# Optimization experiments

Hardware: AMD Instinct MI355X
Metric: run time of the kernel (lower is better)

Reference implementation:

```python
import jax, jax.numpy as jnp
import numpy as np

NEG_SLOPE = 0.2  # PyG GATConv default LeakyReLU slope
EPS = 1e-16


def gat_layer(x, W, a_src, a_dst, bias, src, dst, heads, out_dim, concat):
    N = x.shape[0]
    h = (x @ W).reshape(N, heads, out_dim)          # [N,H,C]
    alpha_src = (h * a_src).sum(-1)                  # [N,H]
    alpha_dst = (h * a_dst).sum(-1)                  # [N,H]
    e = jax.nn.leaky_relu(alpha_src[src] + alpha_dst[dst], NEG_SLOPE)  # [E,H]
    # segment softmax over incoming edges of each destination node
    m = jax.ops.segment_max(e, dst, num_segments=N)  # [N,H]
    p = jnp.exp(e - m[dst])
    denom = jax.ops.segment_sum(p, dst, num_segments=N)
    alpha = p / (denom[dst] + EPS)                   # [E,H]
    # scatter-aggregate messages to destinations
    out = jax.ops.segment_sum(alpha[:, :, None] * h[src], dst, num_segments=N)  # [N,H,C]
    out = out.reshape(N, heads * out_dim) if concat else out.mean(axis=1)
    return out + bias


def setup_inputs() -> dict:
    N, E, F_IN, NC = 100000, 1600000, 512, 10
    key = jax.random.key(0)
    ks = jax.random.split(key, 9)
    return {
        "x": jax.random.normal(ks[0], (N, F_IN), jnp.float32),
        "W1": jax.random.normal(ks[1], (F_IN, 64), jnp.float32) * (1.0 / np.sqrt(F_IN)),
        "att_src1": jax.random.normal(ks[2], (1, 8, 8), jnp.float32) * 0.1,
        "att_dst1": jax.random.normal(ks[3], (1, 8, 8), jnp.float32) * 0.1,
        "b1": jnp.zeros((64,), jnp.float32),
        "W2": jax.random.normal(ks[4], (64, NC), jnp.float32) * (1.0 / 8.0),
        "att_src2": jax.random.normal(ks[5], (1, 1, NC), jnp.float32) * 0.1,
        "att_dst2": jax.random.normal(ks[6], (1, 1, NC), jnp.float32) * 0.1,
        "b2": jnp.zeros((NC,), jnp.float32),
        "edge_index": jax.random.randint(ks[7], (2, E), 0, N, jnp.int64),
    }


def reference(x, W1, att_src1, att_dst1, b1, W2, att_src2, att_dst2, b2, edge_index):
    N = x.shape[0]
    # add self-loops (PyG GATConv add_self_loops=True default)
    loop = jnp.arange(N, dtype=edge_index.dtype)
    src = jnp.concatenate([edge_index[0], loop])
    dst = jnp.concatenate([edge_index[1], loop])
    h = gat_layer(x, W1, att_src1, att_dst1, b1, src, dst, heads=8, out_dim=8, concat=True)
    h = jax.nn.elu(h)
    nc = W2.shape[1]
    out = gat_layer(h, W2, att_src2, att_dst2, b2, src, dst, heads=1, out_dim=nc, concat=False)
    return jax.nn.log_softmax(out, axis=1)
```

## Files before the change

kernel.cpp:

```cpp
#include <hip/hip_runtime.h>
#include <math.h>

#define NEG 0.2f

typedef __bf16 bf16x8 __attribute__((ext_vector_type(8)));
typedef float  f32x4  __attribute__((ext_vector_type(4)));

__global__ void w1prep_k(const float* __restrict__ W1, __bf16* __restrict__ W1b)
{
    int i = blockIdx.x * 256 + threadIdx.x;
    int n = i & 63;
    int k0 = (i >> 6) * 8;
#pragma unroll
    for (int j = 0; j < 8; ++j)
        W1b[(size_t)i * 8 + j] = (__bf16)W1[(size_t)(k0 + j) * 64 + n];
}

__global__ __launch_bounds__(256, 4) void gemm1_k(const float* __restrict__ x,
                                                  const __bf16* __restrict__ W1b,
                                                  float* __restrict__ h1, int Nn)
{
    int t = threadIdx.x;
    int wave = t >> 6, lane = t & 63;
    int lm = lane & 15, lk = lane >> 4;
    int rowa = blockIdx.x * 64 + wave * 16 + lm;
    const float* xrow = x + (size_t)(rowa < Nn ? rowa : 0) * 512;
    f32x4 acc[4] = {};
#pragma unroll
    for (int ch = 0; ch < 16; ++ch) {
        float4 a0 = *(const float4*)(xrow + ch * 32 + lk * 8);
        float4 a1 = *(const float4*)(xrow + ch * 32 + lk * 8 + 4);
        bf16x8 af;
        af[0] = (__bf16)a0.x; af[1] = (__bf16)a0.y;
        af[2] = (__bf16)a0.z; af[3] = (__bf16)a0.w;
        af[4] = (__bf16)a1.x; af[5] = (__bf16)a1.y;
        af[6] = (__bf16)a1.z; af[7] = (__bf16)a1.w;
#pragma unroll
        for (int nt = 0; nt < 4; ++nt) {
            bf16x8 bf = *(const bf16x8*)(W1b + ((size_t)((ch * 4 + lk) * 64) + nt * 16 + lm) * 8);
            acc[nt] = __builtin_amdgcn_mfma_f32_16x16x32_bf16(af, bf, acc[nt], 0, 0, 0);
        }
    }
    int rowbase = blockIdx.x * 64 + wave * 16 + lk * 4;
#pragma unroll
    for (int nt = 0; nt < 4; ++nt) {
#pragma unroll
        for (int j = 0; j < 4; ++j) {
            int gr = rowbase + j;
            if (gr < Nn) h1[(size_t)gr * 64 + nt * 16 + lm] = acc[nt][j];
        }
    }
}

__global__ void attn1_k(const float* __restrict__ h1, const float* __restrict__ asrc,
                        const float* __restrict__ adst, float* __restrict__ as1,
                        float* __restrict__ ad1, int Nn)
{
    int tid = blockIdx.x * 256 + threadIdx.x;
    if (tid >= Nn * 8) return;
    int n = tid >> 3, h = tid & 7;
    const float* hp = h1 + (size_t)n * 64 + h * 8;
    float s = 0.f, d = 0.f;
#pragma unroll
    for (int c = 0; c < 8; ++c) {
        float v = hp[c];
        s += v * asrc[h * 8 + c];
        d += v * adst[h * 8 + c];
    }
    as1[tid] = s;
    ad1[tid] = d;
}

__global__ void hist_rank_k(const int* __restrict__ ei, int E, int Nn,
                            int* __restrict__ deg, int* __restrict__ rank)
{
    int e = blockIdx.x * 256 + threadIdx.x;
    int Ep = E + Nn;
    if (e >= Ep) return;
    int d = (e < E) ? ei[E + e] : e - E;
    rank[e] = atomicAdd(&deg[d], 1);
}

__global__ void scan_a_k(const int* __restrict__ deg, int Nn, int* __restrict__ bsum)
{
    __shared__ int tmp[256];
    int t = threadIdx.x;
    int base = blockIdx.x * 1024 + t * 4;
    int s = 0;
#pragma unroll
    for (int j = 0; j < 4; ++j) { int i = base + j; if (i < Nn) s += deg[i]; }
    tmp[t] = s;
    __syncthreads();
    for (int off = 1; off < 256; off <<= 1) {
        int a = (t >= off) ? tmp[t - off] : 0;
        __syncthreads();
        tmp[t] += a;
        __syncthreads();
    }
    if (t == 255) bsum[blockIdx.x] = tmp[255];
}

__global__ void scan_b_k(int* __restrict__ bsum, int nb)
{
    __shared__ int tmp[256];
    int t = threadIdx.x;
    int v = (t < nb) ? bsum[t] : 0;
    tmp[t] = v;
    __syncthreads();
    for (int off = 1; off < 256; off <<= 1) {
        int a = (t >= off) ? tmp[t - off] : 0;
        __syncthreads();
        tmp[t] += a;
        __syncthreads();
    }
    if (t < nb) bsum[t] = tmp[t] - v;
}

__global__ void scan_c_k(const int* __restrict__ deg, int Nn, const int* __restrict__ boff,
                         int* __restrict__ rowptr)
{
    __shared__ int tmp[256];
    int t = threadIdx.x;
    int base = blockIdx.x * 1024 + t * 4;
    int v[4];
    int s = 0;
#pragma unroll
    for (int j = 0; j < 4; ++j) {
        int i = base + j;
        v[j] = (i < Nn) ? deg[i] : 0;
        s += v[j];
    }
    tmp[t] = s;
    __syncthreads();
    for (int off = 1; off < 256; off <<= 1) {
        int a = (t >= off) ? tmp[t - off] : 0;
        __syncthreads();
        tmp[t] += a;
        __syncthreads();
    }
    int excl = boff[blockIdx.x] + tmp[t] - s;
#pragma unroll
    for (int j = 0; j < 4; ++j) {
        int i = base + j;
        if (i < Nn) {
            rowptr[i] = excl;
            excl += v[j];
            if (i == Nn - 1) rowptr[Nn] = excl;
        }
    }
}

__global__ void scat2_k(const int* __restrict__ ei, int E, int Nn,
                        const int* __restrict__ rowptr, const int* __restrict__ rank,
                        int* __restrict__ csr)
{
    int e = blockIdx.x * 256 + threadIdx.x;
    int Ep = E + Nn;
    if (e >= Ep) return;
    int s, d;
    if (e < E) { s = ei[e]; d = ei[E + e]; } else { s = d = e - E; }
    csr[rowptr[d] + rank[e]] = s;
}

__global__ __launch_bounds__(256) void agg1_k(const int* __restrict__ csr,
                                              const int* __restrict__ rowptr,
                                              const float* __restrict__ as1,
                                              const float* __restrict__ ad1,
                                              const float* __restrict__ h1,
                                              float* __restrict__ out1, int Nn)
{
    int wid = (blockIdx.x * 256 + threadIdx.x) >> 6;
    if (wid >= Nn) return;
    int lane = threadIdx.x & 63;
    int sub = lane >> 4;
    int c4 = lane & 15;
    int h = c4 >> 1;
    float adv = ad1[wid * 8 + h];
    int start = rowptr[wid];
    int len = rowptr[wid + 1] - start;
    float accp = 0.f;
    float4 accv = make_float4(0.f, 0.f, 0.f, 0.f);
    int i = sub;
    for (; i + 12 < len; i += 16) {
        int s0 = csr[start + i];
        int s1 = csr[start + i + 4];
        int s2 = csr[start + i + 8];
        int s3 = csr[start + i + 12];
        float e0 = as1[s0 * 8 + h] + adv;
        float e1 = as1[s1 * 8 + h] + adv;
        float e2 = as1[s2 * 8 + h] + adv;
        float e3 = as1[s3 * 8 + h] + adv;
        float4 hv0 = *(const float4*)(h1 + (size_t)s0 * 64 + c4 * 4);
        float4 hv1 = *(const float4*)(h1 + (size_t)s1 * 64 + c4 * 4);
        float4 hv2 = *(const float4*)(h1 + (size_t)s2 * 64 + c4 * 4);
        float4 hv3 = *(const float4*)(h1 + (size_t)s3 * 64 + c4 * 4);
        e0 = e0 > 0.f ? e0 : NEG * e0;
        e1 = e1 > 0.f ? e1 : NEG * e1;
        e2 = e2 > 0.f ? e2 : NEG * e2;
        e3 = e3 > 0.f ? e3 : NEG * e3;
        float p0 = __expf(e0), p1 = __expf(e1), p2 = __expf(e2), p3 = __expf(e3);
        accp += (p0 + p1) + (p2 + p3);
        accv.x += p0 * hv0.x + p1 * hv1.x + p2 * hv2.x + p3 * hv3.x;
        accv.y += p0 * hv0.y + p1 * hv1.y + p2 * hv2.y + p3 * hv3.y;
        accv.z += p0 * hv0.z + p1 * hv1.z + p2 * hv2.z + p3 * hv3.z;
        accv.w += p0 * hv0.w + p1 * hv1.w + p2 * hv2.w + p3 * hv3.w;
    }
    for (; i < len; i += 4) {
        int s0 = csr[start + i];
        float e0 = as1[s0 * 8 + h] + adv;
        float4 hv0 = *(const float4*)(h1 + (size_t)s0 * 64 + c4 * 4);
        e0 = e0 > 0.f ? e0 : NEG * e0;
        float p0 = __expf(e0);
        accp += p0;
        accv.x += p0 * hv0.x;
        accv.y += p0 * hv0.y;
        accv.z += p0 * hv0.z;
        accv.w += p0 * hv0.w;
    }
    accp   += __shfl_xor(accp, 16);
    accv.x += __shfl_xor(accv.x, 16);
    accv.y += __shfl_xor(accv.y, 16);
    accv.z += __shfl_xor(accv.z, 16);
    accv.w += __shfl_xor(accv.w, 16);
    accp   += __shfl_xor(accp, 32);
    accv.x += __shfl_xor(accv.x, 32);
    accv.y += __shfl_xor(accv.y, 32);
    accv.z += __shfl_xor(accv.z, 32);
    accv.w += __shfl_xor(accv.w, 32);
    if (sub == 0) {
        float inv = 1.f / (accp + 1e-16f);
        float4 o = make_float4(accv.x * inv, accv.y * inv, accv.z * inv, accv.w * inv);
        *(float4*)(out1 + (size_t)wid * 64 + c4 * 4) = o;
    }
}

__global__ void node2_k(const float* __restrict__ out1, const float* __restrict__ b1,
                        const float* __restrict__ W2, const float* __restrict__ as2w,
                        const float* __restrict__ ad2w, float* __restrict__ h2,
                        float* __restrict__ as2, float* __restrict__ ad2, int Nn)
{
    int n = blockIdx.x * 256 + threadIdx.x;
    if (n >= Nn) return;
    float g[64];
#pragma unroll
    for (int c = 0; c < 16; ++c) {
        float4 v = *(const float4*)(out1 + (size_t)n * 64 + c * 4);
        float4 b = *(const float4*)(b1 + c * 4);
        float t0 = v.x + b.x, t1 = v.y + b.y, t2 = v.z + b.z, t3 = v.w + b.w;
        g[c * 4 + 0] = t0 > 0.f ? t0 : expm1f(t0);
        g[c * 4 + 1] = t1 > 0.f ? t1 : expm1f(t1);
        g[c * 4 + 2] = t2 > 0.f ? t2 : expm1f(t2);
        g[c * 4 + 3] = t3 > 0.f ? t3 : expm1f(t3);
    }
    float acc[10] = {};
#pragma unroll
    for (int k = 0; k < 64; ++k) {
#pragma unroll
        for (int j = 0; j < 10; ++j) acc[j] += g[k] * W2[k * 10 + j];
    }
    float s = 0.f, d = 0.f;
#pragma unroll
    for (int j = 0; j < 10; ++j) {
        h2[(size_t)n * 16 + j] = acc[j];
        s += acc[j] * as2w[j];
        d += acc[j] * ad2w[j];
    }
    as2[n] = s;
    ad2[n] = d;
}

__global__ __launch_bounds__(256) void agg2_k(const int* __restrict__ csr,
                                              const int* __restrict__ rowptr,
                                              const float* __restrict__ as2,
                                              const float* __restrict__ ad2,
                                              const float* __restrict__ h2,
                                              float* __restrict__ out, int Nn)
{
    int wid = (blockIdx.x * 256 + threadIdx.x) >> 6;
    if (wid >= Nn) return;
    int lane = threadIdx.x & 63;
    int sub = lane >> 4;
    int c = lane & 15;
    float adv = ad2[wid];
    int start = rowptr[wid];
    int len = rowptr[wid + 1] - start;
    float accp = 0.f, accv = 0.f;
    int i = sub;
    for (; i + 12 < len; i += 16) {
        int s0 = csr[start + i];
        int s1 = csr[start + i + 4];
        int s2 = csr[start + i + 8];
        int s3 = csr[start + i + 12];
        float e0 = as2[s0] + adv;
        float e1 = as2[s1] + adv;
        float e2 = as2[s2] + adv;
        float e3 = as2[s3] + adv;
        float v0 = (c < 10) ? h2[(size_t)s0 * 16 + c] : 0.f;
        float v1 = (c < 10) ? h2[(size_t)s1 * 16 + c] : 0.f;
        float v2 = (c < 10) ? h2[(size_t)s2 * 16 + c] : 0.f;
        float v3 = (c < 10) ? h2[(size_t)s3 * 16 + c] : 0.f;
        e0 = e0 > 0.f ? e0 : NEG * e0;
        e1 = e1 > 0.f ? e1 : NEG * e1;
        e2 = e2 > 0.f ? e2 : NEG * e2;
        e3 = e3 > 0.f ? e3 : NEG * e3;
        float p0 = __expf(e0), p1 = __expf(e1), p2 = __expf(e2), p3 = __expf(e3);
        accp += (p0 + p1) + (p2 + p3);
        accv += p0 * v0 + p1 * v1 + p2 * v2 + p3 * v3;
    }
    for (; i < len; i += 4) {
        int s0 = csr[start + i];
        float e0 = as2[s0] + adv;
        float v0 = (c < 10) ? h2[(size_t)s0 * 16 + c] : 0.f;
        e0 = e0 > 0.f ? e0 : NEG * e0;
        float p0 = __expf(e0);
        accp += p0;
        accv += p0 * v0;
    }
    accp += __shfl_xor(accp, 16);
    accv += __shfl_xor(accv, 16);
    accp += __shfl_xor(accp, 32);
    accv += __shfl_xor(accv, 32);
    if (sub == 0 && c < 10)
        out[(size_t)wid * 10 + c] = accv / (accp + 1e-16f);
}

__global__ void lsm_k(float* __restrict__ out, const float* __restrict__ b2, int Nn)
{
    int n = blockIdx.x * 256 + threadIdx.x;
    if (n >= Nn) return;
    float z[10];
    float m = -1e30f;
#pragma unroll
    for (int j = 0; j < 10; ++j) {
        z[j] = out[(size_t)n * 10 + j] + b2[j];
        m = fmaxf(m, z[j]);
    }
    float ssum = 0.f;
#pragma unroll
    for (int j = 0; j < 10; ++j) ssum += expf(z[j] - m);
    float lse = m + logf(ssum);
#pragma unroll
    for (int j = 0; j < 10; ++j) out[(size_t)n * 10 + j] = z[j] - lse;
}

extern "C" void kernel_launch(void* const* d_in, const int* in_sizes, int n_in,
                              void* d_out, int out_size, void* d_ws, size_t ws_size,
                              hipStream_t stream)
{
    const float* x     = (const float*)d_in[0];
    const float* W1    = (const float*)d_in[1];
    const float* asrc1 = (const float*)d_in[2];
    const float* adst1 = (const float*)d_in[3];
    const float* b1    = (const float*)d_in[4];
    const float* W2    = (const float*)d_in[5];
    const float* asrc2 = (const float*)d_in[6];
    const float* adst2 = (const float*)d_in[7];
    const float* b2    = (const float*)d_in[8];
    const int*   ei    = (const int*)d_in[9];
    float* out = (float*)d_out;

    int F  = in_sizes[1] / 64;
    int Nn = in_sizes[0] / F;
    int E  = in_sizes[9] / 2;
    int Ep = E + Nn;
    int nb = (Nn + 1023) / 1024;

    float* f = (float*)d_ws;
    __bf16* w1b = (__bf16*)f;  f += 512 * 64 / 2;
    float* h1   = f;  f += (size_t)Nn * 64;
    float* as1  = f;  f += (size_t)Nn * 8;
    float* ad1  = f;  f += (size_t)Nn * 8;
    float* h2   = f;  f += (size_t)Nn * 16;
    float* as2  = f;  f += Nn;
    float* ad2  = f;  f += Nn;
    float* out1 = f;  f += (size_t)Nn * 64;
    int* ip = (int*)f;
    int* deg    = ip;  ip += Nn;
    int* rowptr = ip;  ip += Nn + 1;
    int* bsum   = ip;  ip += 256;
    int* rank   = ip;  ip += Ep;
    int* csr    = ip;  ip += Ep;

    hipMemsetAsync(deg, 0, (size_t)Nn * sizeof(int), stream);
    hist_rank_k<<<(Ep + 255) / 256, 256, 0, stream>>>(ei, E, Nn, deg, rank);
    scan_a_k<<<nb, 256, 0, stream>>>(deg, Nn, bsum);
    scan_b_k<<<1, 256, 0, stream>>>(bsum, nb);
    scan_c_k<<<nb, 256, 0, stream>>>(deg, Nn, bsum, rowptr);
    scat2_k<<<(Ep + 255) / 256, 256, 0, stream>>>(ei, E, Nn, rowptr, rank, csr);

    w1prep_k<<<16, 256, 0, stream>>>(W1, w1b);
    gemm1_k<<<(Nn + 63) / 64, 256, 0, stream>>>(x, w1b, h1, Nn);
    attn1_k<<<(Nn * 8 + 255) / 256, 256, 0, stream>>>(h1, asrc1, adst1, as1, ad1, Nn);
    agg1_k<<<(Nn * 64 + 255) / 256, 256, 0, stream>>>(csr, rowptr, as1, ad1, h1, out1, Nn);

    node2_k<<<(Nn + 255) / 256, 256, 0, stream>>>(out1, b1, W2, asrc2, adst2, h2, as2, ad2, Nn);
    agg2_k<<<(Nn * 64 + 255) / 256, 256, 0, stream>>>(csr, rowptr, as2, ad2, h2, out, Nn);
    lsm_k<<<(Nn + 255) / 256, 256, 0, stream>>>(out, b2, Nn);
}
```

Measured before the change: 582.6 us.

## Fuse attention logits into GEMM, node transform into agg1, log-softmax into agg2

Computes the layer-1 attention logits in the GEMM epilogue with lane shuffles, and folds bias, ELU, the W2 projection and the layer-2 logits into the end of the layer-1 aggregation kernel. It also moves log-softmax into the layer-2 aggregation kernel. CSR building now uses a cursor atomic in the scatter instead of storing per-edge ranks. Together this drops three kernel launches and the out1 and rank buffers. In exchange the aggregation kernel does more work per wave, and the scatter order within each row becomes nondeterministic.

```diff
diff --git a/kernel.cpp b/kernel.cpp
--- a/kernel.cpp
+++ b/kernel.cpp
@@ -16,9 +16,13 @@
         W1b[(size_t)i * 8 + j] = (__bf16)W1[(size_t)(k0 + j) * 64 + n];
 }
 
-__global__ __launch_bounds__(256, 4) void gemm1_k(const float* __restrict__ x,
-                                                  const __bf16* __restrict__ W1b,
-                                                  float* __restrict__ h1, int Nn)
+__global__ __launch_bounds__(256, 4) void gemm1a_k(const float* __restrict__ x,
+                                                   const __bf16* __restrict__ W1b,
+                                                   const float* __restrict__ asrc,
+                                                   const float* __restrict__ adst,
+                                                   float* __restrict__ h1,
+                                                   float* __restrict__ as1,
+                                                   float* __restrict__ ad1, int Nn)
 {
     int t = threadIdx.x;
     int wave = t >> 6, lane = t & 63;
@@ -50,35 +54,34 @@
             if (gr < Nn) h1[(size_t)gr * 64 + nt * 16 + lm] = acc[nt][j];
         }
     }
-}
-
-__global__ void attn1_k(const float* __restrict__ h1, const float* __restrict__ asrc,
-                        const float* __restrict__ adst, float* __restrict__ as1,
-                        float* __restrict__ ad1, int Nn)
-{
-    int tid = blockIdx.x * 256 + threadIdx.x;
-    if (tid >= Nn * 8) return;
-    int n = tid >> 3, h = tid & 7;
-    const float* hp = h1 + (size_t)n * 64 + h * 8;
-    float s = 0.f, d = 0.f;
-#pragma unroll
-    for (int c = 0; c < 8; ++c) {
-        float v = hp[c];
-        s += v * asrc[h * 8 + c];
-        d += v * adst[h * 8 + c];
-    }
-    as1[tid] = s;
-    ad1[tid] = d;
-}
-
-__global__ void hist_rank_k(const int* __restrict__ ei, int E, int Nn,
-                            int* __restrict__ deg, int* __restrict__ rank)
+#pragma unroll
+    for (int nt = 0; nt < 4; ++nt) {
+        float ws = asrc[nt * 16 + lm];
+        float wd = adst[nt * 16 + lm];
+#pragma unroll
+        for (int j = 0; j < 4; ++j) {
+            float sv = acc[nt][j] * ws;
+            float dv = acc[nt][j] * wd;
+            sv += __shfl_xor(sv, 1); dv += __shfl_xor(dv, 1);
+            sv += __shfl_xor(sv, 2); dv += __shfl_xor(dv, 2);
+            sv += __shfl_xor(sv, 4); dv += __shfl_xor(dv, 4);
+            int gr = rowbase + j;
+            if ((lm & 7) == 0 && gr < Nn) {
+                int hh = nt * 2 + (lm >> 3);
+                as1[(size_t)gr * 8 + hh] = sv;
+                ad1[(size_t)gr * 8 + hh] = dv;
+            }
+        }
+    }
+}
+
+__global__ void hist_k(const int* __restrict__ ei, int E, int Nn, int* __restrict__ deg)
 {
     int e = blockIdx.x * 256 + threadIdx.x;
     int Ep = E + Nn;
     if (e >= Ep) return;
     int d = (e < E) ? ei[E + e] : e - E;
-    rank[e] = atomicAdd(&deg[d], 1);
+    atomicAdd(&deg[d], 1);
 }
 
 __global__ void scan_a_k(const int* __restrict__ deg, int Nn, int* __restrict__ bsum)
@@ -117,7 +120,7 @@
 }
 
 __global__ void scan_c_k(const int* __restrict__ deg, int Nn, const int* __restrict__ boff,
-                         int* __restrict__ rowptr)
+                         int* __restrict__ rowptr, int* __restrict__ cur)
 {
     __shared__ int tmp[256];
     int t = threadIdx.x;
@@ -144,31 +147,42 @@
         int i = base + j;
         if (i < Nn) {
             rowptr[i] = excl;
+            cur[i] = excl;
             excl += v[j];
             if (i == Nn - 1) rowptr[Nn] = excl;
         }
     }
 }
 
-__global__ void scat2_k(const int* __restrict__ ei, int E, int Nn,
-                        const int* __restrict__ rowptr, const int* __restrict__ rank,
-                        int* __restrict__ csr)
+__global__ void scat_k(const int* __restrict__ ei, int E, int Nn,
+                       int* __restrict__ cur, int* __restrict__ csr)
 {
     int e = blockIdx.x * 256 + threadIdx.x;
     int Ep = E + Nn;
     if (e >= Ep) return;
     int s, d;
     if (e < E) { s = ei[e]; d = ei[E + e]; } else { s = d = e - E; }
-    csr[rowptr[d] + rank[e]] = s;
-}
-
-__global__ __launch_bounds__(256) void agg1_k(const int* __restrict__ csr,
-                                              const int* __restrict__ rowptr,
-                                              const float* __restrict__ as1,
-                                              const float* __restrict__ ad1,
-                                              const float* __restrict__ h1,
-                                              float* __restrict__ out1, int Nn)
-{
+    int pos = atomicAdd(&cur[d], 1);
+    csr[pos] = s;
+}
+
+__global__ __launch_bounds__(256) void agg1n_k(const int* __restrict__ csr,
+                                               const int* __restrict__ rowptr,
+                                               const float* __restrict__ as1,
+                                               const float* __restrict__ ad1,
+                                               const float* __restrict__ h1,
+                                               const float* __restrict__ b1,
+                                               const float* __restrict__ W2,
+                                               const float* __restrict__ as2w,
+                                               const float* __restrict__ ad2w,
+                                               float* __restrict__ h2,
+                                               float* __restrict__ as2,
+                                               float* __restrict__ ad2, int Nn)
+{
+    __shared__ float W2s[640];
+    for (int i = threadIdx.x; i < 640; i += 256) W2s[i] = W2[i];
+    __syncthreads();
+
     int wid = (blockIdx.x * 256 + threadIdx.x) >> 6;
     if (wid >= Nn) return;
     int lane = threadIdx.x & 63;
@@ -227,54 +241,44 @@
     accv.y += __shfl_xor(accv.y, 32);
     accv.z += __shfl_xor(accv.z, 32);
     accv.w += __shfl_xor(accv.w, 32);
-    if (sub == 0) {
-        float inv = 1.f / (accp + 1e-16f);
-        float4 o = make_float4(accv.x * inv, accv.y * inv, accv.z * inv, accv.w * inv);
-        *(float4*)(out1 + (size_t)wid * 64 + c4 * 4) = o;
-    }
-}
-
-__global__ void node2_k(const float* __restrict__ out1, const float* __restrict__ b1,
-                        const float* __restrict__ W2, const float* __restrict__ as2w,
-                        const float* __restrict__ ad2w, float* __restrict__ h2,
-                        float* __restrict__ as2, float* __restrict__ ad2, int Nn)
-{
-    int n = blockIdx.x * 256 + threadIdx.x;
-    if (n >= Nn) return;
-    float g[64];
-#pragma unroll
-    for (int c = 0; c < 16; ++c) {
-        float4 v = *(const float4*)(out1 + (size_t)n * 64 + c * 4);
-        float4 b = *(const float4*)(b1 + c * 4);
-        float t0 = v.x + b.x, t1 = v.y + b.y, t2 = v.z + b.z, t3 = v.w + b.w;
-        g[c * 4 + 0] = t0 > 0.f ? t0 : expm1f(t0);
-        g[c * 4 + 1] = t1 > 0.f ? t1 : expm1f(t1);
-        g[c * 4 + 2] = t2 > 0.f ? t2 : expm1f(t2);
-        g[c * 4 + 3] = t3 > 0.f ? t3 : expm1f(t3);
-    }
-    float acc[10] = {};
-#pragma unroll
-    for (int k = 0; k < 64; ++k) {
-#pragma unroll
-        for (int j = 0; j < 10; ++j) acc[j] += g[k] * W2[k * 10 + j];
-    }
-    float s = 0.f, d = 0.f;
-#pragma unroll
-    for (int j = 0; j < 10; ++j) {
-        h2[(size_t)n * 16 + j] = acc[j];
-        s += acc[j] * as2w[j];
-        d += acc[j] * ad2w[j];
-    }
-    as2[n] = s;
-    ad2[n] = d;
-}
-
-__global__ __launch_bounds__(256) void agg2_k(const int* __restrict__ csr,
-                                              const int* __restrict__ rowptr,
-                                              const float* __restrict__ as2,
-                                              const float* __restrict__ ad2,
-                                              const float* __restrict__ h2,
-                                              float* __restrict__ out, int Nn)
+
+    float inv = 1.f / (accp + 1e-16f);
+    float4 b = *(const float4*)(b1 + c4 * 4);
+    float g0 = accv.x * inv + b.x; g0 = g0 > 0.f ? g0 : expm1f(g0);
+    float g1 = accv.y * inv + b.y; g1 = g1 > 0.f ? g1 : expm1f(g1);
+    float g2 = accv.z * inv + b.z; g2 = g2 > 0.f ? g2 : expm1f(g2);
+    float g3 = accv.w * inv + b.w; g3 = g3 > 0.f ? g3 : expm1f(g3);
+    int k0 = c4 * 4;
+    float aj[10];
+#pragma unroll
+    for (int j = 0; j < 10; ++j)
+        aj[j] = g0 * W2s[(k0 + 0) * 10 + j] + g1 * W2s[(k0 + 1) * 10 + j]
+              + g2 * W2s[(k0 + 2) * 10 + j] + g3 * W2s[(k0 + 3) * 10 + j];
+#pragma unroll
+    for (int m = 1; m <= 8; m <<= 1) {
+#pragma unroll
+        for (int j = 0; j < 10; ++j) aj[j] += __shfl_xor(aj[j], m);
+    }
+    if (lane == 0) {
+        float s2 = 0.f, d2 = 0.f;
+#pragma unroll
+        for (int j = 0; j < 10; ++j) { s2 += aj[j] * as2w[j]; d2 += aj[j] * ad2w[j]; }
+        *(float4*)(h2 + (size_t)wid * 16 + 0) = make_float4(aj[0], aj[1], aj[2], aj[3]);
+        *(float4*)(h2 + (size_t)wid * 16 + 4) = make_float4(aj[4], aj[5], aj[6], aj[7]);
+        h2[(size_t)wid * 16 + 8] = aj[8];
+        h2[(size_t)wid * 16 + 9] = aj[9];
+        as2[wid] = s2;
+        ad2[wid] = d2;
+    }
+}
+
+__global__ __launch_bounds__(256) void agg2l_k(const int* __restrict__ csr,
+                                               const int* __restrict__ rowptr,
+                                               const float* __restrict__ as2,
+                                               const float* __restrict__ ad2,
+                                               const float* __restrict__ h2,
+                                               const float* __restrict__ b2,
+                                               float* __restrict__ out, int Nn)
 {
     int wid = (blockIdx.x * 256 + threadIdx.x) >> 6;
     if (wid >= Nn) return;
@@ -320,27 +324,21 @@
     accv += __shfl_xor(accv, 16);
     accp += __shfl_xor(accp, 32);
     accv += __shfl_xor(accv, 32);
+
+    float z = (c < 10) ? accv / (accp + 1e-16f) + b2[c] : -1e30f;
+    float m = z;
+    m = fmaxf(m, __shfl_xor(m, 1));
+    m = fmaxf(m, __shfl_xor(m, 2));
+    m = fmaxf(m, __shfl_xor(m, 4));
+    m = fmaxf(m, __shfl_xor(m, 8));
+    float p = (c < 10) ? expf(z - m) : 0.f;
+    p += __shfl_xor(p, 1);
+    p += __shfl_xor(p, 2);
+    p += __shfl_xor(p, 4);
+    p += __shfl_xor(p, 8);
+    float lse = m + logf(p);
     if (sub == 0 && c < 10)
-        out[(size_t)wid * 10 + c] = accv / (accp + 1e-16f);
-}
-
-__global__ void lsm_k(float* __restrict__ out, const float* __restrict__ b2, int Nn)
-{
-    int n = blockIdx.x * 256 + threadIdx.x;
-    if (n >= Nn) return;
-    float z[10];
-    float m = -1e30f;
-#pragma unroll
-    for (int j = 0; j < 10; ++j) {
-        z[j] = out[(size_t)n * 10 + j] + b2[j];
-        m = fmaxf(m, z[j]);
-    }
-    float ssum = 0.f;
-#pragma unroll
-    for (int j = 0; j < 10; ++j) ssum += expf(z[j] - m);
-    float lse = m + logf(ssum);
-#pragma unroll
-    for (int j = 0; j < 10; ++j) out[(size_t)n * 10 + j] = z[j] - lse;
+        out[(size_t)wid * 10 + c] = z - lse;
 }
 
 extern "C" void kernel_launch(void* const* d_in, const int* in_sizes, int n_in,
@@ -373,27 +371,25 @@
     float* h2   = f;  f += (size_t)Nn * 16;
     float* as2  = f;  f += Nn;
     float* ad2  = f;  f += Nn;
-    float* out1 = f;  f += (size_t)Nn * 64;
     int* ip = (int*)f;
     int* deg    = ip;  ip += Nn;
     int* rowptr = ip;  ip += Nn + 1;
     int* bsum   = ip;  ip += 256;
-    int* rank   = ip;  ip += Ep;
+    int* cur    = ip;  ip += Nn;
     int* csr    = ip;  ip += Ep;
 
     hipMemsetAsync(deg, 0, (size_t)Nn * sizeof(int), stream);
-    hist_rank_k<<<(Ep + 255) / 256, 256, 0, stream>>>(ei, E, Nn, deg, rank);
+    hist_k<<<(Ep + 255) / 256, 256, 0, stream>>>(ei, E, Nn, deg);
     scan_a_k<<<nb, 256, 0, stream>>>(deg, Nn, bsum);
     scan_b_k<<<1, 256, 0, stream>>>(bsum, nb);
-    scan_c_k<<<nb, 256, 0, stream>>>(deg, Nn, bsum, rowptr);
-    scat2_k<<<(Ep + 255) / 256, 256, 0, stream>>>(ei, E, Nn, rowptr, rank, csr);
+    scan_c_k<<<nb, 256, 0, stream>>>(deg, Nn, bsum, rowptr, cur);
+    scat_k<<<(Ep + 255) / 256, 256, 0, stream>>>(ei, E, Nn, cur, csr);
 
     w1prep_k<<<16, 256, 0, stream>>>(W1, w1b);
-    gemm1_k<<<(Nn + 63) / 64, 256, 0, stream>>>(x, w1b, h1, Nn);
-    attn1_k<<<(Nn * 8 + 255) / 256, 256, 0, stream>>>(h1, asrc1, adst1, as1, ad1, Nn);
-    agg1_k<<<(Nn * 64 + 255) / 256, 256, 0, stream>>>(csr, rowptr, as1, ad1, h1, out1, Nn);
-
-    node2_k<<<(Nn + 255) / 256, 256, 0, stream>>>(out1, b1, W2, asrc2, adst2, h2, as2, ad2, Nn);
-    agg2_k<<<(Nn * 64 + 255) / 256, 256, 0, stream>>>(csr, rowptr, as2, ad2, h2, out, Nn);
-    lsm_k<<<(Nn + 255) / 256, 256, 0, stream>>>(out, b2, Nn);
-}
+    gemm1a_k<<<(Nn + 63) / 64, 256, 0, stream>>>(x, w1b, asrc1, adst1, h1, as1, ad1, Nn);
+
+    agg1n_k<<<(Nn + 3) / 4, 256, 0, stream>>>(csr, rowptr, as1, ad1, h1,
+                                              b1, W2, asrc2, adst2, h2, as2, ad2, Nn);
+
+    agg2l_k<<<(Nn + 3) / 4, 256, 0, stream>>>(csr, rowptr, as2, ad2, h2, b2, out, Nn);
+}
```

Result: slower. 670.2 us (+15.0%).
